# Kernel optimization log

Measured on AMD Instinct MI355X. Metric: run time of the kernel, lower is better.

## Reference

```python
import jax, jax.numpy as jnp
import numpy as np

HEADS = 16
ROT_DIM = 32  # RotaryEmbedding(dim=32), interleaved (GPT-J style) as in rotary_embedding_torch
THETA = 10000.0


def _rope(x):
    # x: (B, H, S, hd); rotate first ROT_DIM dims, pass through the rest
    S = x.shape[-2]
    inv_freq = 1.0 / (THETA ** (jnp.arange(0, ROT_DIM, 2, dtype=jnp.float32) / ROT_DIM))  # (ROT_DIM/2,)
    ang = jnp.arange(S, dtype=jnp.float32)[:, None] * inv_freq[None, :]                   # (S, ROT_DIM/2)
    ang = jnp.repeat(ang, 2, axis=-1)                                                     # (S, ROT_DIM) interleaved
    cos, sin = jnp.cos(ang), jnp.sin(ang)
    xr, xp = x[..., :ROT_DIM], x[..., ROT_DIM:]
    # rotate_half, interleaved pairs: (x1, x2) -> (-x2, x1)
    x2 = xr.reshape(*xr.shape[:-1], ROT_DIM // 2, 2)
    xr_half = jnp.stack([-x2[..., 1], x2[..., 0]], axis=-1).reshape(xr.shape)
    xr = xr * cos + xr_half * sin
    return jnp.concatenate([xr, xp], axis=-1)


def _split_heads(x, H):
    # (S, B, D) -> (B, H, S, hd)
    S, B, D = x.shape
    return x.transpose(1, 0, 2).reshape(B, S, H, D // H).transpose(0, 2, 1, 3)


def setup_inputs() -> dict:
    key = jax.random.key(0)
    ks = jax.random.split(key, 11)
    S, B, D = 2048, 2, 1024
    f = lambda k, shp, s=1.0: jax.random.normal(k, shp, dtype=jnp.float32) * s
    return {
        "Q": f(ks[0], (S, B, D)),
        "K": f(ks[1], (S, B, D)),
        "V": f(ks[2], (S, B, D)),
        "Wq": f(ks[3], (D, D), 0.02), "bq": f(ks[4], (D,), 0.02),
        "Wk": f(ks[5], (D, D), 0.02), "bk": f(ks[6], (D,), 0.02),
        "Wv": f(ks[7], (D, D), 0.02), "bv": f(ks[8], (D,), 0.02),
        "Wo": f(ks[9], (D, D), 0.02), "bo": f(ks[10], (D,), 0.02),
    }


def reference(Q, K, V, Wq, bq, Wk, bk, Wv, bv, Wo, bo):
    S, B, D = Q.shape
    H = HEADS
    hd = D // H
    q = _rope(_split_heads(Q @ Wq.T + bq, H))   # (B, H, S, hd)
    k = _rope(_split_heads(K @ Wk.T + bk, H))
    v = _split_heads(V @ Wv.T + bv, H)
    scores = jnp.einsum("bhqd,bhkd->bhqk", q, k) / jnp.sqrt(jnp.float32(hd))
    probs = jax.nn.softmax(scores, axis=-1)
    out = jnp.einsum("bhqk,bhkd->bhqd", probs, v)  # (B, H, S, hd)
    out = out.transpose(0, 2, 1, 3).reshape(B, S, D).transpose(1, 0, 2)  # (S, B, D)
    return out @ Wo.T + bo
```

## Files before the change

### kernel.cpp

```cpp
#include <hip/hip_runtime.h>
#include <hip/hip_bf16.h>
#include <hip/hip_fp16.h>

#define S_LEN  2048
#define BATCH  2
#define DMODEL 1024
#define NHEADS 16
#define HD     64
#define MROWS  4096
#define LD     72

using f16 = _Float16;
typedef __attribute__((ext_vector_type(8))) _Float16 f16x8;
typedef __attribute__((ext_vector_type(4))) _Float16 f16x4;
typedef __attribute__((ext_vector_type(4))) float    f32x4;

__device__ __forceinline__ void gload16(const void* g, void* l)
{
    __builtin_amdgcn_global_load_lds((const __attribute__((address_space(1))) void*)g,
                                     (__attribute__((address_space(3))) void*)l, 16, 0, 0);
}

__global__ __launch_bounds__(256) void rope_table(float* __restrict__ rc, float* __restrict__ rs)
{
    int idx = blockIdx.x * 256 + threadIdx.x;
    int s = idx >> 4, i = idx & 15;
    float inv = powf(10000.0f, -(float)(2 * i) / 32.0f);
    float ang = (float)s * inv;
    rc[idx] = cosf(ang);
    rs[idx] = sinf(ang);
}

__global__ __launch_bounds__(256) void cvt_all(
    const float* __restrict__ Q, const float* __restrict__ K, const float* __restrict__ V,
    const float* __restrict__ Wq, const float* __restrict__ Wk, const float* __restrict__ Wv,
    const float* __restrict__ Wo, f16* __restrict__ dst)
{
    const int z = blockIdx.y;
    const float* src; size_t off; int n8;
    switch (z) {
        case 0:  src = Q;  off = 0;        n8 = 524288; break;
        case 1:  src = K;  off = 4194304;  n8 = 524288; break;
        case 2:  src = V;  off = 8388608;  n8 = 524288; break;
        case 3:  src = Wq; off = 12582912; n8 = 131072; break;
        case 4:  src = Wk; off = 13631488; n8 = 131072; break;
        case 5:  src = Wv; off = 14680064; n8 = 131072; break;
        default: src = Wo; off = 15728640; n8 = 131072; break;
    }
    int i = blockIdx.x * 256 + threadIdx.x;
    if (i >= n8) return;
    const float4* s = reinterpret_cast<const float4*>(src) + (size_t)i * 2;
    float4 v0 = s[0], v1 = s[1];
    f16x8 h = { (f16)v0.x, (f16)v0.y, (f16)v0.z, (f16)v0.w,
                (f16)v1.x, (f16)v1.y, (f16)v1.z, (f16)v1.w };
    reinterpret_cast<f16x8*>(dst + off)[i] = h;
}

__global__ __launch_bounds__(256) void proj_gemm_h(
    const f16* __restrict__ Xq, const f16* __restrict__ Xk, const f16* __restrict__ Xv,
    const f16* __restrict__ Wq, const f16* __restrict__ Wk, const f16* __restrict__ Wv,
    const float* __restrict__ bq, const float* __restrict__ bk, const float* __restrict__ bv,
    f16* __restrict__ qo, f16* __restrict__ ko, f16* __restrict__ vo,
    const float* __restrict__ rc, const float* __restrict__ rs)
{
    const int mode = blockIdx.z;
    const f16* X     = (mode == 0) ? Xq : (mode == 1) ? Xk : Xv;
    const f16* W     = (mode == 0) ? Wq : (mode == 1) ? Wk : Wv;
    const float* bias = (mode == 0) ? bq : (mode == 1) ? bk : bv;

    __shared__ f16 Al[128 * 32];
    __shared__ f16 Bl[128 * 32];

    const int t = threadIdx.x, lane = t & 63, wid = t >> 6;
    const int q15 = lane & 15, g = lane >> 4;
    const int wr = wid >> 1, wc = wid & 1;
    const int m0 = blockIdx.x * 128, n0 = blockIdx.y * 128;

    const int srow = wid * 16 + (lane >> 2);
    const int scol = (lane & 3) * 8;
    const f16* Xg = X + (size_t)(m0 + srow) * DMODEL + scol;
    const f16* Wg = W + (size_t)(n0 + srow) * DMODEL + scol;
    f16* al0 = &Al[(wid * 16) * 32];
    f16* al1 = &Al[(wid * 16 + 64) * 32];
    f16* bl0 = &Bl[(wid * 16) * 32];
    f16* bl1 = &Bl[(wid * 16 + 64) * 32];

    f32x4 acc[4][4];
    #pragma unroll
    for (int m = 0; m < 4; m++)
        #pragma unroll
        for (int n = 0; n < 4; n++)
            acc[m][n] = f32x4{0.f, 0.f, 0.f, 0.f};

    for (int k0 = 0; k0 < DMODEL; k0 += 32) {
        __syncthreads();
        gload16(Xg + k0, al0);
        gload16(Xg + (size_t)64 * DMODEL + k0, al1);
        gload16(Wg + k0, bl0);
        gload16(Wg + (size_t)64 * DMODEL + k0, bl1);
        __syncthreads();

        f16x8 a[4], b[4];
        #pragma unroll
        for (int m = 0; m < 4; m++)
            a[m] = *reinterpret_cast<const f16x8*>(&Al[(wr * 64 + m * 16 + q15) * 32 + g * 8]);
        #pragma unroll
        for (int n = 0; n < 4; n++)
            b[n] = *reinterpret_cast<const f16x8*>(&Bl[(wc * 64 + n * 16 + q15) * 32 + g * 8]);
        #pragma unroll
        for (int m = 0; m < 4; m++)
            #pragma unroll
            for (int n = 0; n < 4; n++)
                acc[m][n] = __builtin_amdgcn_mfma_f32_16x16x32_f16(a[m], b[n], acc[m][n], 0, 0, 0);
    }

    const int rowb = m0 + wr * 64, colb = n0 + wc * 64;
    #pragma unroll
    for (int n = 0; n < 4; n++) {
        int cN = colb + n * 16 + q15;
        float bvv = bias[cN];
        int h = cN >> 6, d = cN & 63;
        #pragma unroll
        for (int m = 0; m < 4; m++) {
            #pragma unroll
            for (int rg = 0; rg < 4; rg++) {
                int r = rowb + m * 16 + g * 4 + rg;
                int s = r >> 1, bi = r & 1;
                float val = acc[m][n][rg] + bvv;
                if (mode < 2) {
                    float pv = __shfl_xor(val, 1);
                    if (d < 32) {
                        int fi = d >> 1;
                        float cc = rc[s * 16 + fi], ss = rs[s * 16 + fi];
                        val = ((d & 1) == 0) ? val * cc - pv * ss : val * cc + pv * ss;
                    }
                    if (mode == 0) val *= 0.18033688f;
                    ((mode == 0) ? qo : ko)[(((size_t)bi * NHEADS + h) * S_LEN + s) * HD + d] = (f16)val;
                } else {
                    vo[(((size_t)bi * NHEADS + h) * HD + d) * S_LEN + s] = (f16)val;
                }
            }
        }
    }
}

__global__ __launch_bounds__(256) void out_gemm_h(
    const f16* __restrict__ X, const f16* __restrict__ W,
    const float* __restrict__ bias, float* __restrict__ out)
{
    __shared__ f16 Al[128 * 32];
    __shared__ f16 Bl[128 * 32];

    const int t = threadIdx.x, lane = t & 63, wid = t >> 6;
    const int q15 = lane & 15, g = lane >> 4;
    const int wr = wid >> 1, wc = wid & 1;
    const int m0 = blockIdx.x * 128, n0 = blockIdx.y * 128;

    const int srow = wid * 16 + (lane >> 2);
    const int scol = (lane & 3) * 8;
    const f16* Xg = X + (size_t)(m0 + srow) * DMODEL + scol;
    const f16* Wg = W + (size_t)(n0 + srow) * DMODEL + scol;
    f16* al0 = &Al[(wid * 16) * 32];
    f16* al1 = &Al[(wid * 16 + 64) * 32];
    f16* bl0 = &Bl[(wid * 16) * 32];
    f16* bl1 = &Bl[(wid * 16 + 64) * 32];

    f32x4 acc[4][4];
    #pragma unroll
    for (int m = 0; m < 4; m++)
        #pragma unroll
        for (int n = 0; n < 4; n++)
            acc[m][n] = f32x4{0.f, 0.f, 0.f, 0.f};

    for (int k0 = 0; k0 < DMODEL; k0 += 32) {
        __syncthreads();
        gload16(Xg + k0, al0);
        gload16(Xg + (size_t)64 * DMODEL + k0, al1);
        gload16(Wg + k0, bl0);
        gload16(Wg + (size_t)64 * DMODEL + k0, bl1);
        __syncthreads();

        f16x8 a[4], b[4];
        #pragma unroll
        for (int m = 0; m < 4; m++)
            a[m] = *reinterpret_cast<const f16x8*>(&Al[(wr * 64 + m * 16 + q15) * 32 + g * 8]);
        #pragma unroll
        for (int n = 0; n < 4; n++)
            b[n] = *reinterpret_cast<const f16x8*>(&Bl[(wc * 64 + n * 16 + q15) * 32 + g * 8]);
        #pragma unroll
        for (int m = 0; m < 4; m++)
            #pragma unroll
            for (int n = 0; n < 4; n++)
                acc[m][n] = __builtin_amdgcn_mfma_f32_16x16x32_f16(a[m], b[n], acc[m][n], 0, 0, 0);
    }

    const int rowb = m0 + wr * 64, colb = n0 + wc * 64;
    #pragma unroll
    for (int n = 0; n < 4; n++) {
        int cN = colb + n * 16 + q15;
        float bvv = bias[cN];
        #pragma unroll
        for (int m = 0; m < 4; m++) {
            #pragma unroll
            for (int rg = 0; rg < 4; rg++) {
                int r = rowb + m * 16 + g * 4 + rg;
                out[(size_t)r * DMODEL + cN] = acc[m][n][rg] + bvv;
            }
        }
    }
}

__global__ __launch_bounds__(256) void proj_gemm(
    const float* __restrict__ Xq, const float* __restrict__ Xk, const float* __restrict__ Xv,
    const float* __restrict__ Wq, const float* __restrict__ Wk, const float* __restrict__ Wv,
    const float* __restrict__ bq, const float* __restrict__ bk, const float* __restrict__ bv,
    f16* __restrict__ qo, f16* __restrict__ ko, f16* __restrict__ vo,
    const float* __restrict__ rc, const float* __restrict__ rs)
{
    const int mode = blockIdx.z;
    const float* X    = (mode == 0) ? Xq : (mode == 1) ? Xk : Xv;
    const float* W    = (mode == 0) ? Wq : (mode == 1) ? Wk : Wv;
    const float* bias = (mode == 0) ? bq : (mode == 1) ? bk : bv;

    __shared__ f16 Al[128 * 40];
    __shared__ f16 Bl[128 * 40];

    const int t = threadIdx.x;
    const int lane = t & 63, wid = t >> 6;
    const int wr = wid >> 1, wc = wid & 1;
    const int m0 = blockIdx.x * 128, n0 = blockIdx.y * 128;

    f32x4 acc[4][4];
    #pragma unroll
    for (int m = 0; m < 4; m++)
        #pragma unroll
        for (int n = 0; n < 4; n++)
            acc[m][n] = f32x4{0.f, 0.f, 0.f, 0.f};

    for (int k0 = 0; k0 < DMODEL; k0 += 32) {
        __syncthreads();
        #pragma unroll
        for (int i = 0; i < 2; i++) {
            int e = (i * 256 + t) * 8;
            int r = e >> 5, c = e & 31;
            {
                const float* src = &X[(size_t)(m0 + r) * DMODEL + k0 + c];
                float4 v0 = *reinterpret_cast<const float4*>(src);
                float4 v1 = *reinterpret_cast<const float4*>(src + 4);
                f16x8 h = { (f16)v0.x, (f16)v0.y, (f16)v0.z, (f16)v0.w,
                            (f16)v1.x, (f16)v1.y, (f16)v1.z, (f16)v1.w };
                *reinterpret_cast<f16x8*>(&Al[r * 40 + c]) = h;
            }
            {
                const float* src = &W[(size_t)(n0 + r) * DMODEL + k0 + c];
                float4 v0 = *reinterpret_cast<const float4*>(src);
                float4 v1 = *reinterpret_cast<const float4*>(src + 4);
                f16x8 h = { (f16)v0.x, (f16)v0.y, (f16)v0.z, (f16)v0.w,
                            (f16)v1.x, (f16)v1.y, (f16)v1.z, (f16)v1.w };
                *reinterpret_cast<f16x8*>(&Bl[r * 40 + c]) = h;
            }
        }
        __syncthreads();
        f16x8 a[4], b[4];
        #pragma unroll
        for (int m = 0; m < 4; m++)
            a[m] = *reinterpret_cast<const f16x8*>(&Al[(wr * 64 + m * 16 + (lane & 15)) * 40 + (lane >> 4) * 8]);
        #pragma unroll
        for (int n = 0; n < 4; n++)
            b[n] = *reinterpret_cast<const f16x8*>(&Bl[(wc * 64 + n * 16 + (lane & 15)) * 40 + (lane >> 4) * 8]);
        #pragma unroll
        for (int m = 0; m < 4; m++)
            #pragma unroll
            for (int n = 0; n < 4; n++)
                acc[m][n] = __builtin_amdgcn_mfma_f32_16x16x32_f16(a[m], b[n], acc[m][n], 0, 0, 0);
    }

    const int rowb = m0 + wr * 64, colb = n0 + wc * 64;
    #pragma unroll
    for (int n = 0; n < 4; n++) {
        int cN = colb + n * 16 + (lane & 15);
        float bvv = bias[cN];
        int h = cN >> 6, d = cN & 63;
        #pragma unroll
        for (int m = 0; m < 4; m++) {
            #pragma unroll
            for (int rg = 0; rg < 4; rg++) {
                int r = rowb + m * 16 + (lane >> 4) * 4 + rg;
                int s = r >> 1, bi = r & 1;
                float val = acc[m][n][rg] + bvv;
                if (mode < 2) {
                    float pv = __shfl_xor(val, 1);
                    if (d < 32) {
                        int fi = d >> 1;
                        float cc = rc[s * 16 + fi], ss = rs[s * 16 + fi];
                        val = ((d & 1) == 0) ? val * cc - pv * ss : val * cc + pv * ss;
                    }
                    if (mode == 0) val *= 0.18033688f;
                    ((mode == 0) ? qo : ko)[(((size_t)bi * NHEADS + h) * S_LEN + s) * HD + d] = (f16)val;
                } else {
                    vo[(((size_t)bi * NHEADS + h) * HD + d) * S_LEN + s] = (f16)val;
                }
            }
        }
    }
}

__global__ __launch_bounds__(256) void out_gemm(
    const f16* __restrict__ X, const float* __restrict__ W,
    const float* __restrict__ bias, float* __restrict__ out)
{
    __shared__ f16 Al[128 * 40];
    __shared__ f16 Bl[128 * 40];

    const int t = threadIdx.x;
    const int lane = t & 63, wid = t >> 6;
    const int wr = wid >> 1, wc = wid & 1;
    const int m0 = blockIdx.x * 128, n0 = blockIdx.y * 128;

    f32x4 acc[4][4];
    #pragma unroll
    for (int m = 0; m < 4; m++)
        #pragma unroll
        for (int n = 0; n < 4; n++)
            acc[m][n] = f32x4{0.f, 0.f, 0.f, 0.f};

    for (int k0 = 0; k0 < DMODEL; k0 += 32) {
        __syncthreads();
        #pragma unroll
        for (int i = 0; i < 2; i++) {
            int e = (i * 256 + t) * 8;
            int r = e >> 5, c = e & 31;
            *reinterpret_cast<uint4*>(&Al[r * 40 + c]) =
                *reinterpret_cast<const uint4*>(&X[(size_t)(m0 + r) * DMODEL + k0 + c]);
            {
                const float* src = &W[(size_t)(n0 + r) * DMODEL + k0 + c];
                float4 v0 = *reinterpret_cast<const float4*>(src);
                float4 v1 = *reinterpret_cast<const float4*>(src + 4);
                f16x8 h = { (f16)v0.x, (f16)v0.y, (f16)v0.z, (f16)v0.w,
                            (f16)v1.x, (f16)v1.y, (f16)v1.z, (f16)v1.w };
                *reinterpret_cast<f16x8*>(&Bl[r * 40 + c]) = h;
            }
        }
        __syncthreads();
        f16x8 a[4], b[4];
        #pragma unroll
        for (int m = 0; m < 4; m++)
            a[m] = *reinterpret_cast<const f16x8*>(&Al[(wr * 64 + m * 16 + (lane & 15)) * 40 + (lane >> 4) * 8]);
        #pragma unroll
        for (int n = 0; n < 4; n++)
            b[n] = *reinterpret_cast<const f16x8*>(&Bl[(wc * 64 + n * 16 + (lane & 15)) * 40 + (lane >> 4) * 8]);
        #pragma unroll
        for (int m = 0; m < 4; m++)
            #pragma unroll
            for (int n = 0; n < 4; n++)
                acc[m][n] = __builtin_amdgcn_mfma_f32_16x16x32_f16(a[m], b[n], acc[m][n], 0, 0, 0);
    }

    const int rowb = m0 + wr * 64, colb = n0 + wc * 64;
    #pragma unroll
    for (int n = 0; n < 4; n++) {
        int cN = colb + n * 16 + (lane & 15);
        float bvv = bias[cN];
        #pragma unroll
        for (int m = 0; m < 4; m++) {
            #pragma unroll
            for (int rg = 0; rg < 4; rg++) {
                int r = rowb + m * 16 + (lane >> 4) * 4 + rg;
                out[(size_t)r * DMODEL + cN] = acc[m][n][rg] + bvv;
            }
        }
    }
}

__global__ __launch_bounds__(512) void attn_fwd(
    const f16* __restrict__ qb, const f16* __restrict__ kb,
    const f16* __restrict__ vt, f16* __restrict__ ctx)
{
    __shared__ f16 Kl[64 * LD];
    __shared__ f16 Vl[64 * LD];
    __shared__ f16 Pl[8 * 16 * LD];

    const int t = threadIdx.x, lane = t & 63, wid = t >> 6;
    const int q15 = lane & 15, g = lane >> 4;
    const int bh = blockIdx.y;
    const int q0 = blockIdx.x * 128 + wid * 16;

    const f16* qptr = qb + ((size_t)bh * S_LEN + q0) * HD;
    f16x8 qf0 = *reinterpret_cast<const f16x8*>(&qptr[q15 * HD + g * 8]);
    f16x8 qf1 = *reinterpret_cast<const f16x8*>(&qptr[q15 * HD + g * 8 + 32]);

    f32x4 ctxa[4];
    #pragma unroll
    for (int i = 0; i < 4; i++) ctxa[i] = f32x4{0.f, 0.f, 0.f, 0.f};
    float mrun = -3.0e38f, lrun = 0.f;

    const int r_st = t >> 3, c_st = (t & 7) * 8;
    const f16* kg = kb + (size_t)bh * S_LEN * HD + (size_t)r_st * HD + c_st;
    const f16* vg = vt + (size_t)bh * HD * S_LEN + (size_t)r_st * S_LEN + c_st;
    f16* kl_st = &Kl[r_st * LD + c_st];
    f16* vl_st = &Vl[r_st * LD + c_st];
    f16* pbase = &Pl[wid * (16 * LD)];

    for (int kt = 0; kt < S_LEN / 64; kt++) {
        __syncthreads();
        *reinterpret_cast<uint4*>(kl_st) = *reinterpret_cast<const uint4*>(kg);
        *reinterpret_cast<uint4*>(vl_st) = *reinterpret_cast<const uint4*>(vg);
        kg += 64 * HD;
        vg += 64;
        __syncthreads();

        f32x4 sc[4];
        __builtin_amdgcn_s_setprio(1);
        #pragma unroll
        for (int f = 0; f < 4; f++) {
            f16x8 kf0 = *reinterpret_cast<const f16x8*>(&Kl[(f * 16 + q15) * LD + g * 8]);
            f16x8 kf1 = *reinterpret_cast<const f16x8*>(&Kl[(f * 16 + q15) * LD + g * 8 + 32]);
            f32x4 z = {0.f, 0.f, 0.f, 0.f};
            z = __builtin_amdgcn_mfma_f32_16x16x32_f16(kf0, qf0, z, 0, 0, 0);
            sc[f] = __builtin_amdgcn_mfma_f32_16x16x32_f16(kf1, qf1, z, 0, 0, 0);
        }
        __builtin_amdgcn_s_setprio(0);

        float pmf[4];
        #pragma unroll
        for (int f = 0; f < 4; f++)
            pmf[f] = fmaxf(fmaxf(sc[f][0], sc[f][1]), fmaxf(sc[f][2], sc[f][3]));
        float pmax = fmaxf(fmaxf(pmf[0], pmf[1]), fmaxf(pmf[2], pmf[3]));
        pmax = fmaxf(pmax, __shfl_xor(pmax, 16));
        pmax = fmaxf(pmax, __shfl_xor(pmax, 32));
        float mnew = fmaxf(mrun, pmax);
        float scale = __builtin_amdgcn_exp2f(mrun - mnew);
        float tsum = 0.f;
        #pragma unroll
        for (int f = 0; f < 4; f++)
            #pragma unroll
            for (int rg = 0; rg < 4; rg++) {
                float p = __builtin_amdgcn_exp2f(sc[f][rg] - mnew);
                sc[f][rg] = p;
                tsum += p;
            }
        tsum += __shfl_xor(tsum, 16);
        tsum += __shfl_xor(tsum, 32);
        lrun = lrun * scale + tsum;
        mrun = mnew;
        #pragma unroll
        for (int n = 0; n < 4; n++) {
            ctxa[n][0] *= scale; ctxa[n][1] *= scale;
            ctxa[n][2] *= scale; ctxa[n][3] *= scale;
        }

        #pragma unroll
        for (int f = 0; f < 4; f++) {
            f16x4 pw = { (f16)sc[f][0], (f16)sc[f][1], (f16)sc[f][2], (f16)sc[f][3] };
            *reinterpret_cast<f16x4*>(&pbase[q15 * LD + f * 16 + g * 4]) = pw;
        }
        asm volatile("s_waitcnt lgkmcnt(0)" ::: "memory");
        __builtin_amdgcn_sched_barrier(0);

        __builtin_amdgcn_s_setprio(1);
        #pragma unroll
        for (int c = 0; c < 2; c++) {
            f16x8 pfr = *reinterpret_cast<const f16x8*>(&pbase[q15 * LD + g * 8 + c * 32]);
            #pragma unroll
            for (int n = 0; n < 4; n++) {
                f16x8 vf = *reinterpret_cast<const f16x8*>(&Vl[(n * 16 + q15) * LD + g * 8 + c * 32]);
                ctxa[n] = __builtin_amdgcn_mfma_f32_16x16x32_f16(vf, pfr, ctxa[n], 0, 0, 0);
            }
        }
        __builtin_amdgcn_s_setprio(0);
    }

    const int bi = bh >> 4, h = bh & 15;
    const int s = q0 + q15;
    float inv = 1.0f / lrun;
    f16* outp = &ctx[((size_t)s * BATCH + bi) * DMODEL + h * HD];
    #pragma unroll
    for (int n = 0; n < 4; n++) {
        f16x4 o = { (f16)(ctxa[n][0] * inv), (f16)(ctxa[n][1] * inv),
                    (f16)(ctxa[n][2] * inv), (f16)(ctxa[n][3] * inv) };
        *reinterpret_cast<f16x4*>(&outp[n * 16 + g * 4]) = o;
    }
}

extern "C" void kernel_launch(void* const* d_in, const int* in_sizes, int n_in,
                              void* d_out, int out_size, void* d_ws, size_t ws_size,
                              hipStream_t stream)
{
    const float* Q  = (const float*)d_in[0];
    const float* K  = (const float*)d_in[1];
    const float* V  = (const float*)d_in[2];
    const float* Wq = (const float*)d_in[3];
    const float* bq = (const float*)d_in[4];
    const float* Wk = (const float*)d_in[5];
    const float* bk = (const float*)d_in[6];
    const float* Wv = (const float*)d_in[7];
    const float* bv = (const float*)d_in[8];
    const float* Wo = (const float*)d_in[9];
    const float* bo = (const float*)d_in[10];
    float* out = (float*)d_out;

    char* w = (char*)d_ws;
    const size_t MBc = 1024 * 1024;
    const size_t NEED_FAST = 56 * MBc + 256 * 1024;

    if (ws_size >= NEED_FAST) {
        f16* cvtb = (f16*)w;
        f16* Xqh = cvtb;
        f16* Xkh = cvtb + 4194304;
        f16* Xvh = cvtb + 8388608;
        f16* Wqh = cvtb + 12582912;
        f16* Wkh = cvtb + 13631488;
        f16* Wvh = cvtb + 14680064;
        f16* Woh = cvtb + 15728640;
        float* rc = (float*)(w + 32 * MBc);
        float* rs = rc + 32768;
        f16* qbuf = (f16*)(w + 32 * MBc + 256 * 1024);
        f16* kbuf = qbuf + 4194304;
        f16* vtb  = kbuf + 4194304;
        f16* ctxb = Xqh;

        rope_table<<<(S_LEN * 16) / 256, 256, 0, stream>>>(rc, rs);
        cvt_all<<<dim3(2048, 7), 256, 0, stream>>>(Q, K, V, Wq, Wk, Wv, Wo, cvtb);
        proj_gemm_h<<<dim3(MROWS / 128, DMODEL / 128, 3), 256, 0, stream>>>(
            Xqh, Xkh, Xvh, Wqh, Wkh, Wvh, bq, bk, bv, qbuf, kbuf, vtb, rc, rs);
        attn_fwd<<<dim3(S_LEN / 128, BATCH * NHEADS), 512, 0, stream>>>(qbuf, kbuf, vtb, ctxb);
        out_gemm_h<<<dim3(MROWS / 128, DMODEL / 128), 256, 0, stream>>>(ctxb, Woh, bo, out);
    } else {
        const size_t szT = (size_t)S_LEN * 16 * sizeof(float);
        const size_t szQ = (size_t)MROWS * DMODEL * sizeof(f16);
        float* rc  = (float*)(w);
        float* rs  = (float*)(w + szT);
        f16* qbuf = (f16*)(w + 2 * szT);
        f16* kbuf = (f16*)(w + 2 * szT + szQ);
        f16* vtb  = (f16*)(w + 2 * szT + 2 * szQ);
        f16* ctxb = (f16*)(w + 2 * szT + 3 * szQ);

        rope_table<<<(S_LEN * 16) / 256, 256, 0, stream>>>(rc, rs);
        proj_gemm<<<dim3(MROWS / 128, DMODEL / 128, 3), 256, 0, stream>>>(
            Q, K, V, Wq, Wk, Wv, bq, bk, bv, qbuf, kbuf, vtb, rc, rs);
        attn_fwd<<<dim3(S_LEN / 128, BATCH * NHEADS), 512, 0, stream>>>(qbuf, kbuf, vtb, ctxb);
        out_gemm<<<dim3(MROWS / 128, DMODEL / 128), 256, 0, stream>>>(ctxb, Wo, bo, out);
    }
}
```

Baseline: 158.9 us.

## Double-buffer attention K/V tiles with async LDS loads and XOR swizzle

Each K/V tile is now loaded with direct global-to-LDS loads into one of two LDS buffers, so the next tile streams in while the current one is being used for the QK and PV matrix products. The per-iteration barriers drop from two to one. The padded LDS rows are replaced by an XOR-swizzled 64-wide layout to avoid bank conflicts without padding. This relies on the barrier also waiting for the outstanding async loads, and it doubles the LDS used for K and V, which could reduce occupancy.

```diff
diff --git a/kernel.cpp b/kernel.cpp
--- a/kernel.cpp
+++ b/kernel.cpp
@@ -376,12 +376,13 @@
     const f16* __restrict__ qb, const f16* __restrict__ kb,
     const f16* __restrict__ vt, f16* __restrict__ ctx)
 {
-    __shared__ f16 Kl[64 * LD];
-    __shared__ f16 Vl[64 * LD];
+    __shared__ f16 Kl[2][64 * 64];
+    __shared__ f16 Vl[2][64 * 64];
     __shared__ f16 Pl[8 * 16 * LD];
 
     const int t = threadIdx.x, lane = t & 63, wid = t >> 6;
     const int q15 = lane & 15, g = lane >> 4;
+    const int sw = q15 & 7;
     const int bh = blockIdx.y;
     const int q0 = blockIdx.x * 128 + wid * 16;
 
@@ -394,27 +395,32 @@
     for (int i = 0; i < 4; i++) ctxa[i] = f32x4{0.f, 0.f, 0.f, 0.f};
     float mrun = -3.0e38f, lrun = 0.f;
 
-    const int r_st = t >> 3, c_st = (t & 7) * 8;
-    const f16* kg = kb + (size_t)bh * S_LEN * HD + (size_t)r_st * HD + c_st;
-    const f16* vg = vt + (size_t)bh * HD * S_LEN + (size_t)r_st * S_LEN + c_st;
-    f16* kl_st = &Kl[r_st * LD + c_st];
-    f16* vl_st = &Vl[r_st * LD + c_st];
+    const int srow = t >> 3;
+    const int sslot = (t & 7) ^ (srow & 7);
+    const f16* kg = kb + (size_t)bh * S_LEN * HD + (size_t)srow * HD + sslot * 8;
+    const f16* vg = vt + (size_t)bh * HD * S_LEN + (size_t)srow * S_LEN + sslot * 8;
+    const int lds_wbase = wid * 512;
     f16* pbase = &Pl[wid * (16 * LD)];
 
+    gload16(kg, &Kl[0][lds_wbase]);
+    gload16(vg, &Vl[0][lds_wbase]);
+    __syncthreads();
+    int cur = 0;
+
     for (int kt = 0; kt < S_LEN / 64; kt++) {
-        __syncthreads();
-        *reinterpret_cast<uint4*>(kl_st) = *reinterpret_cast<const uint4*>(kg);
-        *reinterpret_cast<uint4*>(vl_st) = *reinterpret_cast<const uint4*>(vg);
-        kg += 64 * HD;
-        vg += 64;
-        __syncthreads();
+        if (kt + 1 < S_LEN / 64) {
+            gload16(kg + (size_t)(kt + 1) * 64 * HD, &Kl[cur ^ 1][lds_wbase]);
+            gload16(vg + (size_t)(kt + 1) * 64,      &Vl[cur ^ 1][lds_wbase]);
+        }
+        const f16* Kc = Kl[cur];
+        const f16* Vc = Vl[cur];
 
         f32x4 sc[4];
         __builtin_amdgcn_s_setprio(1);
         #pragma unroll
         for (int f = 0; f < 4; f++) {
-            f16x8 kf0 = *reinterpret_cast<const f16x8*>(&Kl[(f * 16 + q15) * LD + g * 8]);
-            f16x8 kf1 = *reinterpret_cast<const f16x8*>(&Kl[(f * 16 + q15) * LD + g * 8 + 32]);
+            f16x8 kf0 = *reinterpret_cast<const f16x8*>(&Kc[(f * 16 + q15) * 64 + ((g ^ sw) * 8)]);
+            f16x8 kf1 = *reinterpret_cast<const f16x8*>(&Kc[(f * 16 + q15) * 64 + (((g + 4) ^ sw) * 8)]);
             f32x4 z = {0.f, 0.f, 0.f, 0.f};
             z = __builtin_amdgcn_mfma_f32_16x16x32_f16(kf0, qf0, z, 0, 0, 0);
             sc[f] = __builtin_amdgcn_mfma_f32_16x16x32_f16(kf1, qf1, z, 0, 0, 0);
@@ -463,11 +469,14 @@
             f16x8 pfr = *reinterpret_cast<const f16x8*>(&pbase[q15 * LD + g * 8 + c * 32]);
             #pragma unroll
             for (int n = 0; n < 4; n++) {
-                f16x8 vf = *reinterpret_cast<const f16x8*>(&Vl[(n * 16 + q15) * LD + g * 8 + c * 32]);
+                f16x8 vf = *reinterpret_cast<const f16x8*>(&Vc[(n * 16 + q15) * 64 + (((g + c * 4) ^ sw) * 8)]);
                 ctxa[n] = __builtin_amdgcn_mfma_f32_16x16x32_f16(vf, pfr, ctxa[n], 0, 0, 0);
             }
         }
         __builtin_amdgcn_s_setprio(0);
+
+        __syncthreads();
+        cur ^= 1;
     }
 
     const int bi = bh >> 4, h = bh & 15;
```

Result: no change. 156.4 us (-1.6%).
